# Kernel optimization log

Measured on AMD Instinct MI355X. Metric: run time of the kernel, lower is better.

Reference implementation:

```python
import jax, jax.numpy as jnp
import numpy as np

B, CIN, COUT, H, W = 2, 64, 64, 192, 192
G = 2          # offset groups (region + semantic offset branches concatenated)
KK = 9         # 3x3 kernel taps
CG = CIN // G  # channels per offset group


def conv2d(x, w, b):
    # NCHW, OIHW, stride 1, padding 1 (same as nn.Conv2d(k=3, s=1, p=1))
    y = jax.lax.conv_general_dilated(x, w, (1, 1), ((1, 1), (1, 1)),
                                     dimension_numbers=('NCHW', 'OIHW', 'NCHW'))
    return y + b[None, :, None, None]


def bilinear_gather(x, py, px):
    # x: (B,G,C,H,W); py,px: (B,G,K,H,W) absolute sample coords (float)
    b, g, c, h, w = x.shape
    k = py.shape[2]
    y0 = jnp.floor(py)
    x0 = jnp.floor(px)
    ly = (py - y0)[:, :, None]   # (B,G,1,K,H,W)
    lx = (px - x0)[:, :, None]
    xf = x.reshape(b, g, c, h * w)

    def corner(yi, xi):
        valid = (yi >= 0) & (yi < h) & (xi >= 0) & (xi < w)
        idx = (jnp.clip(yi, 0, h - 1).astype(jnp.int32) * w
               + jnp.clip(xi, 0, w - 1).astype(jnp.int32))          # (B,G,K,H,W)
        idxf = idx.reshape(b, g, k * h * w)
        gat = jax.vmap(jax.vmap(lambda xc, ic: jnp.take(xc, ic, axis=1)))(xf, idxf)
        gat = gat.reshape(b, g, c, k, h, w)
        return gat * valid[:, :, None].astype(x.dtype)

    v00 = corner(y0, x0)
    v01 = corner(y0, x0 + 1)
    v10 = corner(y0 + 1, x0)
    v11 = corner(y0 + 1, x0 + 1)
    return (v00 * (1 - ly) * (1 - lx) + v01 * (1 - ly) * lx
            + v10 * ly * (1 - lx) + v11 * ly * lx)


def setup_inputs() -> dict:
    key = jax.random.key(0)
    ks = jax.random.split(key, 12)
    stdv = 1.0 / np.sqrt(CIN * 9)
    inp = {
        'input': jax.random.normal(ks[0], (B, CIN, H, W), jnp.float32),
        'mask_in': jax.random.uniform(ks[1], (B, 1, H, W), jnp.float32),
        'weight': jax.random.uniform(ks[2], (COUT, CIN, 3, 3), jnp.float32, -stdv, stdv),
        'bias': jnp.zeros((COUT,), jnp.float32),
        'sem_w': jax.random.normal(ks[3], (2 * KK, CIN, 3, 3), jnp.float32) * 0.01,
        'sem_b': jnp.zeros((2 * KK,), jnp.float32),
        'reg_w': jax.random.normal(ks[4], (2 * KK, 1, 3, 3), jnp.float32) * 0.01,
        'reg_b': jnp.zeros((2 * KK,), jnp.float32),
        'm1_w': jax.random.normal(ks[5], (KK, 1, 3, 3), jnp.float32) * 0.1,
        'm1_b': jnp.zeros((KK,), jnp.float32),
        'm2_w': jax.random.normal(ks[6], (KK, CIN, 3, 3), jnp.float32) * 0.1,
        'm2_b': jnp.zeros((KK,), jnp.float32),
    }
    return inp


def reference(input, mask_in, weight, bias, sem_w, sem_b, reg_w, reg_b,
              m1_w, m1_b, m2_w, m2_b):
    f32 = input.dtype
    # --- learned offsets: region (group 0) then semantic (group 1) ---
    region_offset = conv2d(mask_in, reg_w, reg_b)    # (B, 2*9, H, W)
    semantic_offset = conv2d(input, sem_w, sem_b)    # (B, 2*9, H, W)
    offset = jnp.concatenate([region_offset, semantic_offset], axis=1)
    off = offset.reshape(B, G, KK, 2, H, W)          # [..., 0]=dy, [..., 1]=dx
    ky = (jnp.arange(KK) // 3 - 1).astype(f32)[None, None, :, None, None]
    kx = (jnp.arange(KK) % 3 - 1).astype(f32)[None, None, :, None, None]
    gy = jnp.arange(H, dtype=f32)[None, None, None, :, None]
    gx = jnp.arange(W, dtype=f32)[None, None, None, None, :]
    py = off[:, :, :, 0] + gy + ky                   # (B,G,K,H,W)
    px = off[:, :, :, 1] + gx + kx

    # --- update mask: deform conv of repeated mask with all-ones weight (no grad) ---
    # mask repeated over CIN channels -> identical within each offset group, so
    # sample one channel per group and scale: out = 2 (out chans) * CG * sum_{g,k}
    mgrp = jnp.broadcast_to(mask_in[:, None], (B, G, 1, H, W))
    sm = bilinear_gather(mgrp, py, px)               # (B,G,1,K,H,W)
    update_mask = jnp.clip(2.0 * CG * sm.sum(axis=(1, 2, 3)), 0.0, 1.0)[:, None]
    update_mask = jax.lax.stop_gradient(update_mask)  # (B,1,H,W)

    # --- modulation masks ---
    dm1 = jax.nn.sigmoid(conv2d(mask_in, m1_w, m1_b))  # (B,9,H,W) -> group 0
    dm2 = jax.nn.sigmoid(conv2d(input, m2_w, m2_b))    # (B,9,H,W) -> group 1
    dmask = jnp.concatenate([dm1, dm2], axis=1).reshape(B, G, KK, H, W)[:, :, None]

    # --- main modulated deformable conv ---
    xg = input.reshape(B, G, CG, H, W)
    sampled = bilinear_gather(xg, py, px) * dmask    # (B,G,CG,K,H,W)
    wr = weight.reshape(COUT, G, CG, KK)
    raw = jnp.einsum('bgckhw,ogck->bohw', sampled, wr) + bias[None, :, None, None]

    output = raw * update_mask
    return output, update_mask
```

## Files before the change

### kernel.cpp

```cpp
#include <hip/hip_runtime.h>
#include <hip/hip_fp16.h>
#include <math.h>

#define B_  2
#define CIN 64
#define COUT 64
#define H_  192
#define W_  192
#define G_  2
#define KK_ 9
#define CG_ 32
#define HW_ (H_*W_)
#define PIX 32
#define XT_ (W_/PIX)
#define PR_ 7
#define PC_ 38
#define PST 72
#define DSTR 69
#define NB_NHWC (B_ * (HW_ / 64))
#define NB_WT   ((18*4*64*8 + 18*2*64*8) / 256)

typedef __attribute__((ext_vector_type(8))) short bf16x8;
typedef __attribute__((ext_vector_type(8))) _Float16 f16x8;
typedef __attribute__((ext_vector_type(4))) unsigned int u32x4;
typedef __attribute__((ext_vector_type(4))) float f32x4;

static __device__ __forceinline__ short f2h(float f) {
    _Float16 h = (_Float16)f;
    return __builtin_bit_cast(short, h);
}
static __device__ __forceinline__ unsigned pk2hu(float lo, float hi) {
    auto h = __builtin_amdgcn_cvt_pkrtz(lo, hi);
    return __builtin_bit_cast(unsigned, h);
}
static __device__ __forceinline__ short2 pk2h(float lo, float hi) {
    auto h = __builtin_amdgcn_cvt_pkrtz(lo, hi);
    return __builtin_bit_cast(short2, h);
}
static __device__ __forceinline__ __half2 bcl(unsigned u) {
    return __builtin_bit_cast(__half2, (unsigned)((u & 0xffffu) | (u << 16)));
}
static __device__ __forceinline__ __half2 bch(unsigned u) {
    return __builtin_bit_cast(__half2, (unsigned)((u >> 16) | (u & 0xffff0000u)));
}
static __device__ __forceinline__ __half2 H2(unsigned u) {
    return __builtin_bit_cast(__half2, u);
}

__global__ __launch_bounds__(256)
void prep_kernel(const float* __restrict__ in,
                 const float* __restrict__ weight,
                 const float* __restrict__ sem_w,
                 const float* __restrict__ m2_w,
                 short* __restrict__ inpT,
                 short* __restrict__ wbm,
                 short* __restrict__ wbs) {
    __shared__ float t[64][65];
    const int tid = threadIdx.x;
    const int bid = blockIdx.x;
    if (bid < NB_NHWC) {
        const int b = bid / (HW_ / 64);
        const int pix0 = (bid % (HW_ / 64)) * 64;
        const float* src = in + (size_t)b * CIN * HW_ + pix0;
        const int c0 = (tid >> 6) * 16;
        const int p  = tid & 63;
        #pragma unroll
        for (int i = 0; i < 16; ++i)
            t[c0 + i][p] = src[(size_t)(c0 + i) * HW_ + p];
        __syncthreads();
        short* dst = inpT + ((size_t)b * HW_ + pix0) * 64;
        #pragma unroll
        for (int i = 0; i < 2; ++i) {
            int item = i * 256 + tid;
            int pp = item >> 3, oct = item & 7;
            bf16x8 v;
            #pragma unroll
            for (int j = 0; j < 8; j += 2) {
                short2 ss = pk2h(t[oct * 8 + j][pp], t[oct * 8 + j + 1][pp]);
                v[j] = ss.x; v[j + 1] = ss.y;
            }
            *(bf16x8*)&dst[pp * 64 + oct * 8] = v;
        }
        return;
    }
    int i = (bid - NB_NHWC) * 256 + tid;
    if (i < 18 * 4 * 64 * 8) {
        int j = i & 7, lane = (i >> 3) & 63, nt = (i >> 9) & 3, gk = i >> 11;
        int n = lane & 15, q = lane >> 4;
        int o = nt * 16 + n;
        int g = gk / 9, k = gk - g * 9;
        int cin = g * CG_ + q * 8 + j;
        wbm[i] = f2h(weight[(o * CIN + cin) * 9 + k]);
        return;
    }
    int ii = i - 18 * 4 * 64 * 8;
    if (ii >= 18 * 2 * 64 * 8) return;
    int j = ii & 7, lane = (ii >> 3) & 63, nt = (ii >> 9) & 1, s = ii >> 10;
    int t_ = s >> 1, h = s & 1;
    int n = lane & 15, q = lane >> 4;
    int o = nt * 16 + n;
    int c = h * 32 + q * 8 + j;
    float v = 0.f;
    if (o < 18)      v = sem_w[(o * CIN + c) * 9 + t_];
    else if (o < 27) v = m2_w[((o - 18) * CIN + c) * 9 + t_];
    wbs[ii] = f2h(v);
}

#define MSTEP(GK) { \
    const uint2 mw0 = meta_w[(GK) * 32 + n]; \
    const uint2 mw1 = meta_w[(GK) * 32 + 16 + n]; \
    const int i0 = (int)meta_i[(GK) * 32 + n] * PST; \
    const int i1 = (int)meta_i[(GK) * 32 + 16 + n] * PST; \
    const short* pb = patch + team * 32 + q * 8; \
    u32x4 d00 = *(const u32x4*)&pb[i0]; \
    u32x4 d01 = *(const u32x4*)&pb[i0 + PST]; \
    u32x4 d10 = *(const u32x4*)&pb[i0 + PC_ * PST]; \
    u32x4 d11 = *(const u32x4*)&pb[i0 + (PC_ + 1) * PST]; \
    u32x4 e00 = *(const u32x4*)&pb[i1]; \
    u32x4 e01 = *(const u32x4*)&pb[i1 + PST]; \
    u32x4 e10 = *(const u32x4*)&pb[i1 + PC_ * PST]; \
    u32x4 e11 = *(const u32x4*)&pb[i1 + (PC_ + 1) * PST]; \
    __half2 v00 = bcl(mw0.x), v01 = bch(mw0.x), v10 = bcl(mw0.y), v11 = bch(mw0.y); \
    __half2 u00 = bcl(mw1.x), u01 = bch(mw1.x), u10 = bcl(mw1.y), u11 = bch(mw1.y); \
    u32x4 ra, rb; \
    _Pragma("unroll") \
    for (int jj = 0; jj < 4; ++jj) { \
        __half2 s = __hfma2(H2(d00[jj]), v00, __hfma2(H2(d01[jj]), v01, \
                    __hfma2(H2(d10[jj]), v10, __hmul2(H2(d11[jj]), v11)))); \
        ra[jj] = __builtin_bit_cast(unsigned, s); \
        __half2 t = __hfma2(H2(e00[jj]), u00, __hfma2(H2(e01[jj]), u01, \
                    __hfma2(H2(e10[jj]), u10, __hmul2(H2(e11[jj]), u11)))); \
        rb[jj] = __builtin_bit_cast(unsigned, t); \
    } \
    f16x8 a0 = __builtin_bit_cast(f16x8, ra); \
    f16x8 a1 = __builtin_bit_cast(f16x8, rb); \
    f16x8 wb0 = ((const f16x8*)wbm)[((GK) * 4 + 0) * 64 + lane]; \
    f16x8 wb1 = ((const f16x8*)wbm)[((GK) * 4 + 1) * 64 + lane]; \
    f16x8 wb2 = ((const f16x8*)wbm)[((GK) * 4 + 2) * 64 + lane]; \
    f16x8 wb3 = ((const f16x8*)wbm)[((GK) * 4 + 3) * 64 + lane]; \
    ma00 = __builtin_amdgcn_mfma_f32_16x16x32_f16(a0, wb0, ma00, 0, 0, 0); \
    ma01 = __builtin_amdgcn_mfma_f32_16x16x32_f16(a0, wb1, ma01, 0, 0, 0); \
    ma02 = __builtin_amdgcn_mfma_f32_16x16x32_f16(a0, wb2, ma02, 0, 0, 0); \
    ma03 = __builtin_amdgcn_mfma_f32_16x16x32_f16(a0, wb3, ma03, 0, 0, 0); \
    ma10 = __builtin_amdgcn_mfma_f32_16x16x32_f16(a1, wb0, ma10, 0, 0, 0); \
    ma11 = __builtin_amdgcn_mfma_f32_16x16x32_f16(a1, wb1, ma11, 0, 0, 0); \
    ma12 = __builtin_amdgcn_mfma_f32_16x16x32_f16(a1, wb2, ma12, 0, 0, 0); \
    ma13 = __builtin_amdgcn_mfma_f32_16x16x32_f16(a1, wb3, ma13, 0, 0, 0); \
}

#define DUMP() { \
    float* dw = dout + w * (32 * DSTR); \
    _Pragma("unroll") \
    for (int r = 0; r < 4; ++r) { \
        dw[(q * 4 + r) * DSTR +  0 + n] = ma00[r]; \
        dw[(q * 4 + r) * DSTR + 16 + n] = ma01[r]; \
        dw[(q * 4 + r) * DSTR + 32 + n] = ma02[r]; \
        dw[(q * 4 + r) * DSTR + 48 + n] = ma03[r]; \
        dw[(16 + q * 4 + r) * DSTR +  0 + n] = ma10[r]; \
        dw[(16 + q * 4 + r) * DSTR + 16 + n] = ma11[r]; \
        dw[(16 + q * 4 + r) * DSTR + 32 + n] = ma12[r]; \
        dw[(16 + q * 4 + r) * DSTR + 48 + n] = ma13[r]; \
    } \
}

__global__ __launch_bounds__(256)
void fused_kernel(const short* __restrict__ inpT,
                  const float* __restrict__ mask_in,
                  const short* __restrict__ wbs,
                  const short* __restrict__ wbm,
                  const float* __restrict__ sem_b,
                  const float* __restrict__ reg_w, const float* __restrict__ reg_b,
                  const float* __restrict__ m1_w, const float* __restrict__ m1_b,
                  const float* __restrict__ m2_b,
                  const float* __restrict__ bias,
                  float* __restrict__ out, float* __restrict__ um_out) {
    __shared__ __align__(16) short patch[PR_ * PC_ * PST];
    __shared__ __align__(16) float red[2 * 32 * 36];
    __shared__ __align__(8) uint2 meta_w[18 * 32];
    __shared__ unsigned short meta_i[18 * 32];
    __shared__ float ums[4 * 32];
    __shared__ float umv[32];
    float* dout = (float*)patch;

    const int tid  = threadIdx.x;
    const int lane = tid & 63;
    const int w    = __builtin_amdgcn_readfirstlane(tid >> 6);
    const int team = w >> 1;
    const int kh   = w & 1;
    const int n = lane & 15, q = lane >> 4;

    const int bid  = blockIdx.x;
    const int band = bid & 7;
    const int jb   = bid >> 3;
    const int xt   = jb % XT_;
    const int rr   = band * 48 + jb / XT_;
    const int y    = rr % H_;
    const int b    = rr / H_;
    const int x0   = xt * PIX;

    for (int i = tid; i < PR_ * PC_ * 8; i += 256) {
        int chunk = i & 7;
        int cc = (i >> 3) % PC_;
        int rp = (i >> 3) / PC_;
        int yy = y - 3 + rp;
        int xx = x0 - 3 + cc;
        bf16x8 v = {0, 0, 0, 0, 0, 0, 0, 0};
        if (yy >= 0 && yy < H_ && xx >= 0 && xx < W_)
            v = *(const bf16x8*)&inpT[((size_t)(b * HW_ + yy * W_ + xx)) * 64 + chunk * 8];
        *(bf16x8*)&patch[(rp * PC_ + cc) * PST + chunk * 8] = v;
    }
    __syncthreads();

    f32x4 acc0 = {0.f, 0.f, 0.f, 0.f}, acc1 = {0.f, 0.f, 0.f, 0.f};
    for (int ss = 0; ss < 9; ++ss) {
        int s = team * 9 + ss;
        int tt = s >> 1, hh = s & 1;
        int dy = tt / 3 - 1, dx = tt % 3 - 1;
        int r = dy + 3;
        int c = kh * 16 + n + dx + 3;
        f16x8 a = *(const f16x8*)&patch[(r * PC_ + c) * PST + hh * 32 + q * 8];
        f16x8 b0 = ((const f16x8*)wbs)[(s * 2 + 0) * 64 + lane];
        f16x8 b1 = ((const f16x8*)wbs)[(s * 2 + 1) * 64 + lane];
        acc0 = __builtin_amdgcn_mfma_f32_16x16x32_f16(a, b0, acc0, 0, 0, 0);
        acc1 = __builtin_amdgcn_mfma_f32_16x16x32_f16(a, b1, acc1, 0, 0, 0);
    }
    #pragma unroll
    for (int r = 0; r < 4; ++r) {
        red[team * 1152 + (kh * 16 + q * 4 + r) * 36 + n]      = acc0[r];
        red[team * 1152 + (kh * 16 + q * 4 + r) * 36 + 16 + n] = acc1[r];
    }
    __syncthreads();

    {
        const int g    = team;
        const int half = lane >> 5;
        const int pxl  = lane & 31;
        const int xl   = x0 + pxl;
        const int pixl = y * W_ + xl;
        const bool vxm = xl > 0, vxp = (xl + 1) < W_;
        const bool vym = y > 0,  vyp = (y + 1) < H_;
        const int qk = (kh << 1) | half;
        const int k0 = (qk == 0) ? 0 : (qk == 1) ? 3 : (qk == 2) ? 5 : 7;
        const int k1 = (qk == 0) ? 3 : (qk == 1) ? 5 : (qk == 2) ? 7 : 9;
        float off_[18], mm[9];
        if (g == 0) {
            const float* mbp = mask_in + (size_t)b * HW_ + pixl;
            float mv[9];
            mv[0] = (vym && vxm) ? mbp[-W_ - 1] : 0.f;
            mv[1] = vym ? mbp[-W_] : 0.f;
            mv[2] = (vym && vxp) ? mbp[-W_ + 1] : 0.f;
            mv[3] = vxm ? mbp[-1] : 0.f;
            mv[4] = mbp[0];
            mv[5] = vxp ? mbp[1] : 0.f;
            mv[6] = (vyp && vxm) ? mbp[W_ - 1] : 0.f;
            mv[7] = vyp ? mbp[W_] : 0.f;
            mv[8] = (vyp && vxp) ? mbp[W_ + 1] : 0.f;
            #pragma unroll
            for (int o = 0; o < 18; ++o) off_[o] = reg_b[o];
            #pragma unroll
            for (int o = 0; o < 9; ++o) mm[o] = m1_b[o];
            #pragma unroll
            for (int t = 0; t < 9; ++t) {
                float vt = mv[t];
                #pragma unroll
                for (int o = 0; o < 18; ++o) off_[o] += vt * reg_w[o * 9 + t];
                #pragma unroll
                for (int o = 0; o < 9; ++o) mm[o] += vt * m1_w[o * 9 + t];
            }
        } else {
            #pragma unroll
            for (int o = 0; o < 18; ++o)
                off_[o] = red[pxl * 36 + o] + red[1152 + pxl * 36 + o] + sem_b[o];
            #pragma unroll
            for (int o = 0; o < 9; ++o)
                mm[o] = red[pxl * 36 + 18 + o] + red[1152 + pxl * 36 + 18 + o] + m2_b[o];
        }

        const float* mb = mask_in + (size_t)b * HW_;
        float s_um = 0.f;
        #pragma unroll
        for (int k = 0; k < 9; ++k) {
            if (k < k0 || k >= k1) continue;
            float Y = off_[2 * k]     + (float)y  + (float)(k / 3 - 1);
            float X = off_[2 * k + 1] + (float)xl + (float)(k % 3 - 1);
            int gk = g * 9 + k;
            float dm = 1.f / (1.f + __expf(-mm[k]));
            float y0f = floorf(Y), x0f = floorf(X);
            int yi0 = (int)y0f, xi0 = (int)x0f;
            float ly = Y - y0f, lx = X - x0f;
            int yi1 = yi0 + 1, xi1 = xi0 + 1;
            bool vy0 = (yi0 >= 0 && yi0 < H_), vy1 = (yi1 >= 0 && yi1 < H_);
            bool vx0 = (xi0 >= 0 && xi0 < W_), vx1 = (xi1 >= 0 && xi1 < W_);
            float w00f = (vy0 && vx0) ? (1.f - ly) * (1.f - lx) : 0.f;
            float w01f = (vy0 && vx1) ? (1.f - ly) * lx : 0.f;
            float w10f = (vy1 && vx0) ? ly * (1.f - lx) : 0.f;
            float w11f = (vy1 && vx1) ? ly * lx : 0.f;
            int yc0 = min(max(yi0, 0), H_ - 1), yc1 = min(max(yi1, 0), H_ - 1);
            int xc0 = min(max(xi0, 0), W_ - 1), xc1 = min(max(xi1, 0), W_ - 1);
            s_um += w00f * mb[yc0 * W_ + xc0] + w01f * mb[yc0 * W_ + xc1]
                  + w10f * mb[yc1 * W_ + xc0] + w11f * mb[yc1 * W_ + xc1];
            int r0 = min(max(yi0 - (y - 3), 0), PR_ - 2);
            int c0 = min(max(xi0 - (x0 - 3), 0), PC_ - 2);
            meta_w[gk * 32 + pxl] = make_uint2(pk2hu(w00f * dm, w01f * dm),
                                               pk2hu(w10f * dm, w11f * dm));
            meta_i[gk * 32 + pxl] = (unsigned short)(r0 * PC_ + c0);
        }
        s_um += __shfl_xor(s_um, 32);
        if (half == 0) ums[w * 32 + pxl] = s_um;
    }
    __syncthreads();

    f32x4 ma00 = {0.f,0.f,0.f,0.f}, ma01 = {0.f,0.f,0.f,0.f};
    f32x4 ma02 = {0.f,0.f,0.f,0.f}, ma03 = {0.f,0.f,0.f,0.f};
    f32x4 ma10 = {0.f,0.f,0.f,0.f}, ma11 = {0.f,0.f,0.f,0.f};
    f32x4 ma12 = {0.f,0.f,0.f,0.f}, ma13 = {0.f,0.f,0.f,0.f};
    {
        const int t9 = team * 9;
        if (kh == 0) {
            MSTEP(t9 + 0) MSTEP(t9 + 1) MSTEP(t9 + 2) MSTEP(t9 + 3) MSTEP(t9 + 4)
        } else {
            MSTEP(t9 + 5) MSTEP(t9 + 6) MSTEP(t9 + 7) MSTEP(t9 + 8)
        }
    }
    __syncthreads();

    DUMP();
    if (tid < 32) {
        float s = ums[tid] + ums[32 + tid] + ums[64 + tid] + ums[96 + tid];
        float u = fminf(fmaxf(64.f * s, 0.f), 1.f);
        um_out[(size_t)b * HW_ + y * W_ + x0 + tid] = u;
        umv[tid] = u;
    }
    __syncthreads();

    {
        const int pxs = tid & 31;
        const int o0  = (tid >> 5) * 8;
        float u = umv[pxs];
        float* ob = out + ((size_t)b * COUT + o0) * HW_ + y * W_ + x0 + pxs;
        const float* bs = bias + o0;
        const float* dp = dout + pxs * DSTR + o0;
        #pragma unroll
        for (int o = 0; o < 8; ++o)
            ob[(size_t)o * HW_] = (dp[o] + dp[32 * DSTR + o] + dp[2 * 32 * DSTR + o]
                                   + dp[3 * 32 * DSTR + o] + bs[o]) * u;
    }
}

extern "C" void kernel_launch(void* const* d_in, const int* in_sizes, int n_in,
                              void* d_out, int out_size, void* d_ws, size_t ws_size,
                              hipStream_t stream) {
    const float* input   = (const float*)d_in[0];
    const float* mask_in = (const float*)d_in[1];
    const float* weight  = (const float*)d_in[2];
    const float* bias    = (const float*)d_in[3];
    const float* sem_w   = (const float*)d_in[4];
    const float* sem_b   = (const float*)d_in[5];
    const float* reg_w   = (const float*)d_in[6];
    const float* reg_b   = (const float*)d_in[7];
    const float* m1_w    = (const float*)d_in[8];
    const float* m1_b    = (const float*)d_in[9];
    const float* m2_w    = (const float*)d_in[10];
    const float* m2_b    = (const float*)d_in[11];

    float* out = (float*)d_out;
    float* um  = out + (size_t)B_ * COUT * HW_;

    short* inpT = (short*)d_ws;
    short* wbm  = inpT + (size_t)B_ * HW_ * 64;
    short* wbs  = wbm + 18 * 4 * 64 * 8;

    prep_kernel<<<NB_NHWC + NB_WT, 256, 0, stream>>>(
        input, weight, sem_w, m2_w, inpT, wbm, wbs);
    fused_kernel<<<B_ * H_ * XT_, 256, 0, stream>>>(
        inpT, mask_in, wbs, wbm, sem_b, reg_w, reg_b, m1_w, m1_b, m2_b,
        bias, out, um);
}
```

Baseline: 139.5 us.

## Shrink offset reduction buffer to fp16, split offset compute, prefetch gather indices

The semantic-offset reduction buffer now stores fp16 instead of fp32, which halves that shared-memory array. Offset and modulation-mask computation is split between the two kh warps of each team, so each computes only a subset of the outputs. In the main loop, all gather indices and weight loads are issued before the bilinear math, and the update-mask reduction moves earlier into the MFMA phase to overlap with it. The fp16 offsets lose precision in the sampling coordinates, which could change results near pixel boundaries.

```diff
diff --git a/kernel.cpp b/kernel.cpp
--- a/kernel.cpp
+++ b/kernel.cpp
@@ -17,6 +17,7 @@
 #define PC_ 38
 #define PST 72
 #define DSTR 69
+#define RST 38
 #define NB_NHWC (B_ * (HW_ / 64))
 #define NB_WT   ((18*4*64*8 + 18*2*64*8) / 256)
 
@@ -28,6 +29,10 @@
 static __device__ __forceinline__ short f2h(float f) {
     _Float16 h = (_Float16)f;
     return __builtin_bit_cast(short, h);
+}
+static __device__ __forceinline__ float h2f(short s) {
+    _Float16 h = __builtin_bit_cast(_Float16, s);
+    return (float)h;
 }
 static __device__ __forceinline__ unsigned pk2hu(float lo, float hi) {
     auto h = __builtin_amdgcn_cvt_pkrtz(lo, hi);
@@ -106,20 +111,21 @@
     wbs[ii] = f2h(v);
 }
 
-#define MSTEP(GK) { \
+#define MSTEPP(GK, I0, I1) { \
+    f16x8 wb0 = ((const f16x8*)wbm)[((GK) * 4 + 0) * 64 + lane]; \
+    f16x8 wb1 = ((const f16x8*)wbm)[((GK) * 4 + 1) * 64 + lane]; \
+    f16x8 wb2 = ((const f16x8*)wbm)[((GK) * 4 + 2) * 64 + lane]; \
+    f16x8 wb3 = ((const f16x8*)wbm)[((GK) * 4 + 3) * 64 + lane]; \
+    u32x4 d00 = *(const u32x4*)&pb[(I0)]; \
+    u32x4 d01 = *(const u32x4*)&pb[(I0) + PST]; \
+    u32x4 d10 = *(const u32x4*)&pb[(I0) + PC_ * PST]; \
+    u32x4 d11 = *(const u32x4*)&pb[(I0) + (PC_ + 1) * PST]; \
+    u32x4 e00 = *(const u32x4*)&pb[(I1)]; \
+    u32x4 e01 = *(const u32x4*)&pb[(I1) + PST]; \
+    u32x4 e10 = *(const u32x4*)&pb[(I1) + PC_ * PST]; \
+    u32x4 e11 = *(const u32x4*)&pb[(I1) + (PC_ + 1) * PST]; \
     const uint2 mw0 = meta_w[(GK) * 32 + n]; \
     const uint2 mw1 = meta_w[(GK) * 32 + 16 + n]; \
-    const int i0 = (int)meta_i[(GK) * 32 + n] * PST; \
-    const int i1 = (int)meta_i[(GK) * 32 + 16 + n] * PST; \
-    const short* pb = patch + team * 32 + q * 8; \
-    u32x4 d00 = *(const u32x4*)&pb[i0]; \
-    u32x4 d01 = *(const u32x4*)&pb[i0 + PST]; \
-    u32x4 d10 = *(const u32x4*)&pb[i0 + PC_ * PST]; \
-    u32x4 d11 = *(const u32x4*)&pb[i0 + (PC_ + 1) * PST]; \
-    u32x4 e00 = *(const u32x4*)&pb[i1]; \
-    u32x4 e01 = *(const u32x4*)&pb[i1 + PST]; \
-    u32x4 e10 = *(const u32x4*)&pb[i1 + PC_ * PST]; \
-    u32x4 e11 = *(const u32x4*)&pb[i1 + (PC_ + 1) * PST]; \
     __half2 v00 = bcl(mw0.x), v01 = bch(mw0.x), v10 = bcl(mw0.y), v11 = bch(mw0.y); \
     __half2 u00 = bcl(mw1.x), u01 = bch(mw1.x), u10 = bcl(mw1.y), u11 = bch(mw1.y); \
     u32x4 ra, rb; \
@@ -134,10 +140,6 @@
     } \
     f16x8 a0 = __builtin_bit_cast(f16x8, ra); \
     f16x8 a1 = __builtin_bit_cast(f16x8, rb); \
-    f16x8 wb0 = ((const f16x8*)wbm)[((GK) * 4 + 0) * 64 + lane]; \
-    f16x8 wb1 = ((const f16x8*)wbm)[((GK) * 4 + 1) * 64 + lane]; \
-    f16x8 wb2 = ((const f16x8*)wbm)[((GK) * 4 + 2) * 64 + lane]; \
-    f16x8 wb3 = ((const f16x8*)wbm)[((GK) * 4 + 3) * 64 + lane]; \
     ma00 = __builtin_amdgcn_mfma_f32_16x16x32_f16(a0, wb0, ma00, 0, 0, 0); \
     ma01 = __builtin_amdgcn_mfma_f32_16x16x32_f16(a0, wb1, ma01, 0, 0, 0); \
     ma02 = __builtin_amdgcn_mfma_f32_16x16x32_f16(a0, wb2, ma02, 0, 0, 0); \
@@ -147,6 +149,16 @@
     ma12 = __builtin_amdgcn_mfma_f32_16x16x32_f16(a1, wb2, ma12, 0, 0, 0); \
     ma13 = __builtin_amdgcn_mfma_f32_16x16x32_f16(a1, wb3, ma13, 0, 0, 0); \
 }
+
+#define LIDX(GK, S) \
+    const int i0_##S = (int)meta_i[(GK) * 32 + n] * PST; \
+    const int i1_##S = (int)meta_i[(GK) * 32 + 16 + n] * PST;
+
+#define UMRED { if (tid < 32) { \
+    float s_ = ums[tid] + ums[32 + tid] + ums[64 + tid] + ums[96 + tid]; \
+    float u_ = fminf(fmaxf(64.f * s_, 0.f), 1.f); \
+    um_out[(size_t)b * HW_ + y * W_ + x0 + tid] = u_; \
+    umv[tid] = u_; } }
 
 #define DUMP() { \
     float* dw = dout + w * (32 * DSTR); \
@@ -163,6 +175,23 @@
     } \
 }
 
+#define COMPOFF(OL, OH, ML, MH) { \
+    if (g == 0) { \
+        _Pragma("unroll") for (int o = (OL); o < (OH); ++o) off_[o] = reg_b[o]; \
+        _Pragma("unroll") for (int k = (ML); k < (MH); ++k) mm[k] = m1_b[k]; \
+        _Pragma("unroll") for (int t = 0; t < 9; ++t) { \
+            float vt = mv[t]; \
+            _Pragma("unroll") for (int o = (OL); o < (OH); ++o) off_[o] += vt * reg_w[o * 9 + t]; \
+            _Pragma("unroll") for (int k = (ML); k < (MH); ++k) mm[k] += vt * m1_w[k * 9 + t]; \
+        } \
+    } else { \
+        _Pragma("unroll") for (int o = (OL); o < (OH); ++o) \
+            off_[o] = h2f(redh[pxl * RST + o]) + h2f(redh[32 * RST + pxl * RST + o]) + sem_b[o]; \
+        _Pragma("unroll") for (int k = (ML); k < (MH); ++k) \
+            mm[k] = h2f(redh[pxl * RST + 18 + k]) + h2f(redh[32 * RST + pxl * RST + 18 + k]) + m2_b[k]; \
+    } \
+}
+
 __global__ __launch_bounds__(256)
 void fused_kernel(const short* __restrict__ inpT,
                   const float* __restrict__ mask_in,
@@ -175,7 +204,7 @@
                   const float* __restrict__ bias,
                   float* __restrict__ out, float* __restrict__ um_out) {
     __shared__ __align__(16) short patch[PR_ * PC_ * PST];
-    __shared__ __align__(16) float red[2 * 32 * 36];
+    __shared__ __align__(16) short redh[2 * 32 * RST];
     __shared__ __align__(8) uint2 meta_w[18 * 32];
     __shared__ unsigned short meta_i[18 * 32];
     __shared__ float ums[4 * 32];
@@ -226,8 +255,8 @@
     }
     #pragma unroll
     for (int r = 0; r < 4; ++r) {
-        red[team * 1152 + (kh * 16 + q * 4 + r) * 36 + n]      = acc0[r];
-        red[team * 1152 + (kh * 16 + q * 4 + r) * 36 + 16 + n] = acc1[r];
+        redh[team * (32 * RST) + (kh * 16 + q * 4 + r) * RST + n]      = f2h(acc0[r]);
+        redh[team * (32 * RST) + (kh * 16 + q * 4 + r) * RST + 16 + n] = f2h(acc1[r]);
     }
     __syncthreads();
 
@@ -243,9 +272,9 @@
         const int k0 = (qk == 0) ? 0 : (qk == 1) ? 3 : (qk == 2) ? 5 : 7;
         const int k1 = (qk == 0) ? 3 : (qk == 1) ? 5 : (qk == 2) ? 7 : 9;
         float off_[18], mm[9];
+        float mv[9];
         if (g == 0) {
             const float* mbp = mask_in + (size_t)b * HW_ + pixl;
-            float mv[9];
             mv[0] = (vym && vxm) ? mbp[-W_ - 1] : 0.f;
             mv[1] = vym ? mbp[-W_] : 0.f;
             mv[2] = (vym && vxp) ? mbp[-W_ + 1] : 0.f;
@@ -255,26 +284,8 @@
             mv[6] = (vyp && vxm) ? mbp[W_ - 1] : 0.f;
             mv[7] = vyp ? mbp[W_] : 0.f;
             mv[8] = (vyp && vxp) ? mbp[W_ + 1] : 0.f;
-            #pragma unroll
-            for (int o = 0; o < 18; ++o) off_[o] = reg_b[o];
-            #pragma unroll
-            for (int o = 0; o < 9; ++o) mm[o] = m1_b[o];
-            #pragma unroll
-            for (int t = 0; t < 9; ++t) {
-                float vt = mv[t];
-                #pragma unroll
-                for (int o = 0; o < 18; ++o) off_[o] += vt * reg_w[o * 9 + t];
-                #pragma unroll
-                for (int o = 0; o < 9; ++o) mm[o] += vt * m1_w[o * 9 + t];
-            }
-        } else {
-            #pragma unroll
-            for (int o = 0; o < 18; ++o)
-                off_[o] = red[pxl * 36 + o] + red[1152 + pxl * 36 + o] + sem_b[o];
-            #pragma unroll
-            for (int o = 0; o < 9; ++o)
-                mm[o] = red[pxl * 36 + 18 + o] + red[1152 + pxl * 36 + 18 + o] + m2_b[o];
         }
+        if (kh == 0) { COMPOFF(0, 10, 0, 5) } else { COMPOFF(10, 18, 5, 9) }
 
         const float* mb = mask_in + (size_t)b * HW_;
         float s_um = 0.f;
@@ -315,22 +326,27 @@
     f32x4 ma10 = {0.f,0.f,0.f,0.f}, ma11 = {0.f,0.f,0.f,0.f};
     f32x4 ma12 = {0.f,0.f,0.f,0.f}, ma13 = {0.f,0.f,0.f,0.f};
     {
+        const short* pb = patch + team * 32 + q * 8;
         const int t9 = team * 9;
         if (kh == 0) {
-            MSTEP(t9 + 0) MSTEP(t9 + 1) MSTEP(t9 + 2) MSTEP(t9 + 3) MSTEP(t9 + 4)
+            LIDX(t9 + 0, 0) LIDX(t9 + 1, 1) LIDX(t9 + 2, 2) LIDX(t9 + 3, 3) LIDX(t9 + 4, 4)
+            UMRED
+            MSTEPP(t9 + 0, i0_0, i1_0)
+            MSTEPP(t9 + 1, i0_1, i1_1)
+            MSTEPP(t9 + 2, i0_2, i1_2)
+            MSTEPP(t9 + 3, i0_3, i1_3)
+            MSTEPP(t9 + 4, i0_4, i1_4)
         } else {
-            MSTEP(t9 + 5) MSTEP(t9 + 6) MSTEP(t9 + 7) MSTEP(t9 + 8)
+            LIDX(t9 + 5, 0) LIDX(t9 + 6, 1) LIDX(t9 + 7, 2) LIDX(t9 + 8, 3)
+            MSTEPP(t9 + 5, i0_0, i1_0)
+            MSTEPP(t9 + 6, i0_1, i1_1)
+            MSTEPP(t9 + 7, i0_2, i1_2)
+            MSTEPP(t9 + 8, i0_3, i1_3)
         }
     }
     __syncthreads();
 
     DUMP();
-    if (tid < 32) {
-        float s = ums[tid] + ums[32 + tid] + ums[64 + tid] + ums[96 + tid];
-        float u = fminf(fmaxf(64.f * s, 0.f), 1.f);
-        um_out[(size_t)b * HW_ + y * W_ + x0 + tid] = u;
-        umv[tid] = u;
-    }
     __syncthreads();
 
     {
```

Result: faster. 128.8 us (-7.6%).
